# Optimization experiments

Measured on AMD Instinct MI355X. Metric: run time of the kernel, lower is better.

## Reference

```python
import jax, jax.numpy as jnp
import numpy as np

B, S, D = 2, 4096, 768
H = 12
HD = D // H  # 64
SCALE = HD ** -0.5


def setup_inputs() -> dict:
    key = jax.random.key(0)
    ks = jax.random.split(key, 5)
    return {
        "x": jax.random.normal(ks[0], (B, S, D), dtype=jnp.float32),
        "qkv_w": jax.random.normal(ks[1], (D, 3 * D), dtype=jnp.float32) * (D ** -0.5),
        "qkv_b": jax.random.normal(ks[2], (3 * D,), dtype=jnp.float32) * 0.02,
        "proj_w": jax.random.normal(ks[3], (D, D), dtype=jnp.float32) * (D ** -0.5),
        "proj_b": jax.random.normal(ks[4], (D,), dtype=jnp.float32) * 0.02,
    }


def reference(x, qkv_w, qkv_b, proj_w, proj_b):
    b, s, d = x.shape
    qkv = x @ qkv_w + qkv_b                      # [B, S, 3D]
    qkv = qkv.reshape(b, s, 3, H, HD)
    q, k, v = jnp.moveaxis(qkv, 2, 0)            # each [B, S, H, HD]
    q = jnp.swapaxes(q, 1, 2)                    # [B, H, S, HD]
    k = jnp.swapaxes(k, 1, 2)
    v = jnp.swapaxes(v, 1, 2)
    attn = jnp.einsum("bhqd,bhkd->bhqk", q, k) * SCALE  # [B, H, S, S]
    attn = jax.nn.softmax(attn, axis=-1)
    out = jnp.einsum("bhqk,bhkd->bhqd", attn, v)        # [B, H, S, HD]
    out = jnp.swapaxes(out, 1, 2).reshape(b, s, d)      # [B, S, D]
    return out @ proj_w + proj_b
```

## Files before the change

kernel.cpp:

```cpp
#include <hip/hip_runtime.h>

typedef unsigned short u16;
typedef __attribute__((ext_vector_type(8))) short bf16x8;
typedef __attribute__((ext_vector_type(4))) float f32x4;
typedef __attribute__((ext_vector_type(16))) float f32x16;

__device__ __forceinline__ u16 f2bf(float f) {
  union { float f; unsigned u; } v; v.f = f;
  unsigned r = v.u + 0x7fffu + ((v.u >> 16) & 1u);
  return (u16)(r >> 16);
}

__device__ __forceinline__ bf16x8 ld_frag(const char* p) {
  union { uint4 u; bf16x8 v; } t;
  t.u = *(const uint4*)p;
  return t.v;
}

__global__ __launch_bounds__(256) void k_prep(const float* __restrict__ x,
                                              const float* __restrict__ qkv_w,
                                              const float* __restrict__ proj_w,
                                              u16* __restrict__ xb,
                                              u16* __restrict__ wt,
                                              u16* __restrict__ pwt) {
  int bid = blockIdx.x, tid = threadIdx.x;
  if (bid < 6144) {
    int i = bid * 256 + tid;
    float4 v = ((const float4*)x)[i];
    ushort4 o; o.x = f2bf(v.x); o.y = f2bf(v.y); o.z = f2bf(v.z); o.w = f2bf(v.w);
    ((ushort4*)xb)[i] = o;
    return;
  }
  __shared__ float tile[32][33];
  const float* in; u16* out; int R, C, bx, by;
  if (bid < 6144 + 1728) {
    int t = bid - 6144; in = qkv_w; out = wt; R = 768; C = 2304;
    bx = (t % 72) * 32; by = (t / 72) * 32;
  } else {
    int t = bid - 7872; in = proj_w; out = pwt; R = 768; C = 768;
    bx = (t % 24) * 32; by = (t / 24) * 32;
  }
  int tx = tid & 31, ty = tid >> 5;
#pragma unroll
  for (int j = 0; j < 32; j += 8)
    tile[ty + j][tx] = in[(size_t)(by + ty + j) * C + bx + tx];
  __syncthreads();
#pragma unroll
  for (int j = 0; j < 32; j += 8)
    out[(size_t)(bx + ty + j) * R + by + tx] = f2bf(tile[tx][ty + j]);
}

#define GAS(p) ((const __attribute__((address_space(1))) void*)(p))
#define LAS(p) ((__attribute__((address_space(3))) void*)(p))

__global__ __launch_bounds__(256) void k_gemm_qkv(
    const u16* __restrict__ A,
    const u16* __restrict__ Bt,
    const float* __restrict__ bias,
    u16* __restrict__ Qb, u16* __restrict__ Kb, u16* __restrict__ Vb) {
  const int K = 768;
  __shared__ u16 Al[128 * 64];
  __shared__ u16 Bl[128 * 64];
  int tn0 = blockIdx.x * 128, tm0 = blockIdx.y * 128;
  int tid = threadIdx.x, w = tid >> 6, lane = tid & 63;
  int l16 = lane & 15, lg = lane >> 4;
  int wm = (w >> 1) * 64, wn = (w & 1) * 64;
  f32x4 acc[4][4];
#pragma unroll
  for (int fm = 0; fm < 4; ++fm)
#pragma unroll
    for (int fn = 0; fn < 4; ++fn) acc[fm][fn] = (f32x4){0.f, 0.f, 0.f, 0.f};
  int srow = w * 32 + (lane >> 3);
  int scol = (lane & 7) * 8;
  for (int k0 = 0; k0 < K; k0 += 64) {
#pragma unroll
    for (int i = 0; i < 4; ++i) {
      __builtin_amdgcn_global_load_lds(GAS(A + (size_t)(tm0 + srow + i * 8) * K + k0 + scol),
                                       LAS((char*)Al + w * 4096 + i * 1024 + lane * 16), 16, 0, 0);
      __builtin_amdgcn_global_load_lds(GAS(Bt + (size_t)(tn0 + srow + i * 8) * K + k0 + scol),
                                       LAS((char*)Bl + w * 4096 + i * 1024 + lane * 16), 16, 0, 0);
    }
    __syncthreads();
#pragma unroll
    for (int ks = 0; ks < 2; ++ks) {
      bf16x8 af[4], bv[4];
#pragma unroll
      for (int f = 0; f < 4; ++f)
        af[f] = *(const bf16x8*)&Al[(wm + f * 16 + l16) * 64 + lg * 8 + ks * 32];
#pragma unroll
      for (int f = 0; f < 4; ++f)
        bv[f] = *(const bf16x8*)&Bl[(wn + f * 16 + l16) * 64 + lg * 8 + ks * 32];
#pragma unroll
      for (int fm = 0; fm < 4; ++fm)
#pragma unroll
        for (int fn = 0; fn < 4; ++fn)
          acc[fm][fn] = __builtin_amdgcn_mfma_f32_16x16x32_bf16(af[fm], bv[fn], acc[fm][fn], 0, 0, 0);
    }
    __syncthreads();
  }
  int part = tn0 / 768;
  u16* dst = part == 0 ? Qb : (part == 1 ? Kb : Vb);
  float qscale = (part == 0) ? 0.18033688011112042f : 1.0f;
#pragma unroll
  for (int fn = 0; fn < 4; ++fn) {
    int nn = tn0 + wn + fn * 16 + l16;
    float bvs = bias[nn];
    int np = nn - part * 768;
    int hh = np >> 6, hd = np & 63;
#pragma unroll
    for (int fm = 0; fm < 4; ++fm) {
#pragma unroll
      for (int r = 0; r < 4; ++r) {
        int m = tm0 + wm + fm * 16 + lg * 4 + r;
        int bb = m >> 12, s = m & 4095;
        size_t idx;
        if (part == 2) {
          int sp = (s & ~12) | ((s & 8) >> 1) | ((s & 4) << 1);
          idx = (((size_t)(bb * 12 + hh)) * 64 + hd) * 4096 + sp;
        } else {
          idx = (((size_t)(bb * 12 + hh)) * 4096 + s) * 64 + hd;
        }
        dst[idx] = f2bf((acc[fm][fn][r] + bvs) * qscale);
      }
    }
  }
}

__global__ __launch_bounds__(256) void k_gemm_proj(
    const u16* __restrict__ A,
    const u16* __restrict__ Bt,
    const float* __restrict__ bias, float* __restrict__ out) {
  const int K = 768;
  __shared__ u16 Al[128 * 64];
  __shared__ u16 Bl[128 * 64];
  int tn0 = blockIdx.x * 128, tm0 = blockIdx.y * 128;
  int tid = threadIdx.x, w = tid >> 6, lane = tid & 63;
  int l16 = lane & 15, lg = lane >> 4;
  int wm = (w >> 1) * 64, wn = (w & 1) * 64;
  f32x4 acc[4][4];
#pragma unroll
  for (int fm = 0; fm < 4; ++fm)
#pragma unroll
    for (int fn = 0; fn < 4; ++fn) acc[fm][fn] = (f32x4){0.f, 0.f, 0.f, 0.f};
  int srow = w * 32 + (lane >> 3);
  int scol = (lane & 7) * 8;
  for (int k0 = 0; k0 < K; k0 += 64) {
#pragma unroll
    for (int i = 0; i < 4; ++i) {
      __builtin_amdgcn_global_load_lds(GAS(A + (size_t)(tm0 + srow + i * 8) * K + k0 + scol),
                                       LAS((char*)Al + w * 4096 + i * 1024 + lane * 16), 16, 0, 0);
      __builtin_amdgcn_global_load_lds(GAS(Bt + (size_t)(tn0 + srow + i * 8) * K + k0 + scol),
                                       LAS((char*)Bl + w * 4096 + i * 1024 + lane * 16), 16, 0, 0);
    }
    __syncthreads();
#pragma unroll
    for (int ks = 0; ks < 2; ++ks) {
      bf16x8 af[4], bv[4];
#pragma unroll
      for (int f = 0; f < 4; ++f)
        af[f] = *(const bf16x8*)&Al[(wm + f * 16 + l16) * 64 + lg * 8 + ks * 32];
#pragma unroll
      for (int f = 0; f < 4; ++f)
        bv[f] = *(const bf16x8*)&Bl[(wn + f * 16 + l16) * 64 + lg * 8 + ks * 32];
#pragma unroll
      for (int fm = 0; fm < 4; ++fm)
#pragma unroll
        for (int fn = 0; fn < 4; ++fn)
          acc[fm][fn] = __builtin_amdgcn_mfma_f32_16x16x32_bf16(af[fm], bv[fn], acc[fm][fn], 0, 0, 0);
    }
    __syncthreads();
  }
#pragma unroll
  for (int fn = 0; fn < 4; ++fn) {
    int nn = tn0 + wn + fn * 16 + l16;
    float bvs = bias[nn];
#pragma unroll
    for (int fm = 0; fm < 4; ++fm) {
#pragma unroll
      for (int r = 0; r < 4; ++r) {
        int m = tm0 + wm + fm * 16 + lg * 4 + r;
        out[(size_t)m * 768 + nn] = acc[fm][fn][r] + bvs;
      }
    }
  }
}

__global__ __launch_bounds__(256, 3) void k_attn(const u16* __restrict__ Qb,
                                                 const u16* __restrict__ Kb,
                                                 const u16* __restrict__ Vtg,
                                                 u16* __restrict__ Ob) {
  const int S = 4096, NH = 12, D = 768;
  __shared__ u16 Kl[2][64 * 64];
  __shared__ u16 Vl[2][64 * 64];

  int bid0 = blockIdx.x;
  int bid = (bid0 & 7) * 96 + (bid0 >> 3);
  int qp = bid & 31;
  int bh = bid >> 5;
  int b = bh / NH, h = bh % NH;
  int rot = ((bid0 >> 8) * 21) & 63;
  const u16* Qh = Qb + (size_t)bh * S * 64;
  const char* Khc = (const char*)(Kb + (size_t)bh * S * 64);
  const char* Vhc = (const char*)(Vtg + (size_t)bh * 64 * S);

  int tid = threadIdx.x, w = tid >> 6, lane = tid & 63;
  int q31 = lane & 31, hi = lane >> 5;
  int swb = (q31 & 7) << 4;
  int coff = (hi << 4);

  unsigned xoff[4];
#pragma unroll
  for (int ks = 0; ks < 4; ++ks)
    xoff[ks] = (unsigned)(q31 * 128 + ((ks * 32 + coff) ^ swb));

  int r8 = lane >> 3;
  int chs = (lane & 7) ^ r8;
  const char* kSrc = Khc + (size_t)(w * 16 + r8) * 128 + chs * 16;
  const char* vSrc = Vhc + (size_t)(w * 16 + r8) * 8192 + chs * 16;
  char* kDst0 = (char*)&Kl[0][0] + w * 2048 + lane * 16;
  char* vDst0 = (char*)&Vl[0][0] + w * 2048 + lane * 16;

  auto STAGE = [&](int bufi, int kv) {
#pragma unroll
    for (int qq = 0; qq < 2; ++qq) {
      __builtin_amdgcn_global_load_lds(GAS(kSrc + (size_t)kv * 8192 + qq * 1024),
                                       LAS(kDst0 + bufi * 8192 + qq * 1024), 16, 0, 0);
      __builtin_amdgcn_global_load_lds(GAS(vSrc + (size_t)qq * 65536 + (size_t)kv * 128),
                                       LAS(vDst0 + bufi * 8192 + qq * 1024), 16, 0, 0);
    }
  };

  int qbase = qp * 128 + w * 32;
  const u16* qrow = Qh + (size_t)(qbase + q31) * 64;
  bf16x8 qf[4];
#pragma unroll
  for (int ks = 0; ks < 4; ++ks)
    qf[ks] = *(const bf16x8*)(qrow + ks * 16 + hi * 8);

  f32x16 of0, of1, la0, la1;
#pragma unroll
  for (int i = 0; i < 16; ++i) { of0[i] = 0.f; of1[i] = 0.f; la0[i] = 0.f; la1[i] = 0.f; }

  auto TILE = [&](const char* KB, const char* VB) {
    f32x16 s0, s1;
#pragma unroll
    for (int i = 0; i < 16; ++i) { s0[i] = 0.f; s1[i] = 0.f; }
    __builtin_amdgcn_s_setprio(1);
#pragma unroll
    for (int ks = 0; ks < 4; ++ks) {
      bf16x8 kf = ld_frag(KB + xoff[ks]);
      s0 = __builtin_amdgcn_mfma_f32_32x32x16_bf16(kf, qf[ks], s0, 0, 0, 0);
    }
#pragma unroll
    for (int ks = 0; ks < 4; ++ks) {
      bf16x8 kf = ld_frag(KB + 4096 + xoff[ks]);
      s1 = __builtin_amdgcn_mfma_f32_32x32x16_bf16(kf, qf[ks], s1, 0, 0, 0);
    }
    __builtin_amdgcn_s_setprio(0);
#pragma unroll
    for (int i = 0; i < 16; ++i) {
      s0[i] = __builtin_amdgcn_exp2f(s0[i]);
      s1[i] = __builtin_amdgcn_exp2f(s1[i]);
    }
    la0 += s0;
    la1 += s1;
    union U8 { unsigned u[4]; bf16x8 v; };
    bf16x8 pf[4];
#define MK_PF(DST, SS, R0)                                                        \
    { U8 tt;                                                                      \
      asm("v_cvt_pk_bf16_f32 %0,%1,%2" : "=v"(tt.u[0]) : "v"(SS[R0+0]), "v"(SS[R0+1])); \
      asm("v_cvt_pk_bf16_f32 %0,%1,%2" : "=v"(tt.u[1]) : "v"(SS[R0+2]), "v"(SS[R0+3])); \
      asm("v_cvt_pk_bf16_f32 %0,%1,%2" : "=v"(tt.u[2]) : "v"(SS[R0+4]), "v"(SS[R0+5])); \
      asm("v_cvt_pk_bf16_f32 %0,%1,%2" : "=v"(tt.u[3]) : "v"(SS[R0+6]), "v"(SS[R0+7])); \
      DST = tt.v; }
    MK_PF(pf[0], s0, 0); MK_PF(pf[1], s0, 8);
    MK_PF(pf[2], s1, 0); MK_PF(pf[3], s1, 8);
#undef MK_PF
    __builtin_amdgcn_s_setprio(1);
#pragma unroll
    for (int ks = 0; ks < 4; ++ks) {
      bf16x8 vf = ld_frag(VB + xoff[ks]);
      of0 = __builtin_amdgcn_mfma_f32_32x32x16_bf16(vf, pf[ks], of0, 0, 0, 0);
    }
#pragma unroll
    for (int ks = 0; ks < 4; ++ks) {
      bf16x8 vf = ld_frag(VB + 4096 + xoff[ks]);
      of1 = __builtin_amdgcn_mfma_f32_32x32x16_bf16(vf, pf[ks], of1, 0, 0, 0);
    }
    __builtin_amdgcn_s_setprio(0);
  };

  const char* K0 = (const char*)&Kl[0][0];
  const char* K1 = (const char*)&Kl[1][0];
  const char* V0 = (const char*)&Vl[0][0];
  const char* V1 = (const char*)&Vl[1][0];

  STAGE(0, rot);
  __syncthreads();

#pragma unroll 1
  for (int kv = 0; kv < S / 64; kv += 2) {
    STAGE(1, (kv + 1 + rot) & 63);
    TILE(K0, V0);
    __syncthreads();
    if (kv + 2 < S / 64) STAGE(0, (kv + 2 + rot) & 63);
    TILE(K1, V1);
    if (kv + 2 < S / 64) __syncthreads();
  }

  float ts[8];
#pragma unroll
  for (int i = 0; i < 8; ++i) ts[i] = (la0[i] + la0[i + 8]) + (la1[i] + la1[i + 8]);
#pragma unroll
  for (int st = 4; st >= 1; st >>= 1)
#pragma unroll
    for (int i = 0; i < 4; ++i)
      if (i < st) ts[i] += ts[i + st];
  float l_full = ts[0] + __shfl_xor(ts[0], 32, 64);
  float inv = 1.f / l_full;
  int q = qbase + q31;
  u16* orow = Ob + (size_t)(b * S + q) * D + h * 64;
#pragma unroll
  for (int g = 0; g < 4; ++g) {
    ushort4 o0, o1;
    o0.x = f2bf(of0[g * 4 + 0] * inv); o0.y = f2bf(of0[g * 4 + 1] * inv);
    o0.z = f2bf(of0[g * 4 + 2] * inv); o0.w = f2bf(of0[g * 4 + 3] * inv);
    o1.x = f2bf(of1[g * 4 + 0] * inv); o1.y = f2bf(of1[g * 4 + 1] * inv);
    o1.z = f2bf(of1[g * 4 + 2] * inv); o1.w = f2bf(of1[g * 4 + 3] * inv);
    int hd0 = g * 8 + hi * 4;
    *(ushort4*)(orow + hd0) = o0;
    *(ushort4*)(orow + 32 + hd0) = o1;
  }
}

extern "C" void kernel_launch(void* const* d_in, const int* in_sizes, int n_in,
                              void* d_out, int out_size, void* d_ws, size_t ws_size,
                              hipStream_t stream) {
  const float* x      = (const float*)d_in[0];
  const float* qkv_w  = (const float*)d_in[1];
  const float* qkv_b  = (const float*)d_in[2];
  const float* proj_w = (const float*)d_in[3];
  const float* proj_b = (const float*)d_in[4];
  float* out = (float*)d_out;

  u16* ws  = (u16*)d_ws;
  u16* xb  = ws;
  u16* wt  = xb + 8192 * 768;
  u16* pwt = wt + 2304 * 768;
  u16* Qb  = pwt + 768 * 768;
  u16* Kb  = Qb + 24 * 4096 * 64;
  u16* Vt  = Kb + 24 * 4096 * 64;
  u16* Ob  = Vt + 24 * 4096 * 64;

  k_prep<<<8448, 256, 0, stream>>>(x, qkv_w, proj_w, xb, wt, pwt);
  k_gemm_qkv<<<dim3(18, 64), 256, 0, stream>>>(xb, wt, qkv_b, Qb, Kb, Vt);
  k_attn<<<768, 256, 0, stream>>>(Qb, Kb, Vt, Ob);
  k_gemm_proj<<<dim3(6, 64), 256, 0, stream>>>(Ob, pwt, proj_b, out);
}
```

Baseline: 221.6 us.

## Stage QKV epilogue through LDS for coalesced stores; halve proj GEMM M-tile

```diff
diff --git a/kernel.cpp b/kernel.cpp
--- a/kernel.cpp
+++ b/kernel.cpp
@@ -59,8 +59,10 @@
     const float* __restrict__ bias,
     u16* __restrict__ Qb, u16* __restrict__ Kb, u16* __restrict__ Vb) {
   const int K = 768;
-  __shared__ u16 Al[128 * 64];
-  __shared__ u16 Bl[128 * 64];
+  __shared__ __align__(16) char SMEM[34816];
+  u16* Al = (u16*)SMEM;
+  u16* Bl = (u16*)(SMEM + 16384);
+  u16* P  = (u16*)SMEM;
   int tn0 = blockIdx.x * 128, tm0 = blockIdx.y * 128;
   int tid = threadIdx.x, w = tid >> 6, lane = tid & 63;
   int l16 = lane & 15, lg = lane >> 4;
@@ -99,30 +101,59 @@
     __syncthreads();
   }
   int part = tn0 / 768;
-  u16* dst = part == 0 ? Qb : (part == 1 ? Kb : Vb);
   float qscale = (part == 0) ? 0.18033688011112042f : 1.0f;
-#pragma unroll
-  for (int fn = 0; fn < 4; ++fn) {
-    int nn = tn0 + wn + fn * 16 + l16;
-    float bvs = bias[nn];
-    int np = nn - part * 768;
-    int hh = np >> 6, hd = np & 63;
-#pragma unroll
-    for (int fm = 0; fm < 4; ++fm) {
-#pragma unroll
-      for (int r = 0; r < 4; ++r) {
-        int m = tm0 + wm + fm * 16 + lg * 4 + r;
-        int bb = m >> 12, s = m & 4095;
-        size_t idx;
-        if (part == 2) {
-          int sp = (s & ~12) | ((s & 8) >> 1) | ((s & 4) << 1);
-          idx = (((size_t)(bb * 12 + hh)) * 64 + hd) * 4096 + sp;
-        } else {
-          idx = (((size_t)(bb * 12 + hh)) * 4096 + s) * 64 + hd;
+
+  if (part == 2) {
+    int lgp = ((lg & 1) << 3) | ((lg & 2) << 1);
+#pragma unroll
+    for (int fn = 0; fn < 4; ++fn) {
+      int n = wn + fn * 16 + l16;
+      float bvs = bias[tn0 + n];
+#pragma unroll
+      for (int fm = 0; fm < 4; ++fm) {
+        int mp = wm + fm * 16 + lgp;
+        ushort4 hv;
+        hv.x = f2bf(acc[fm][fn][0] + bvs);
+        hv.y = f2bf(acc[fm][fn][1] + bvs);
+        hv.z = f2bf(acc[fm][fn][2] + bvs);
+        hv.w = f2bf(acc[fm][fn][3] + bvs);
+        *(ushort4*)&P[n * 136 + mp] = hv;
+      }
+    }
+    __syncthreads();
+    int n = tid >> 1, mc = tid & 1;
+    int np = (tn0 - 1536) + n;
+    int bh2 = (tm0 >> 12) * 12 + (np >> 6);
+    int hd = np & 63;
+    u16* g = Vb + ((size_t)bh2 * 64 + hd) * 4096 + (tm0 & 4095) + mc * 64;
+    const u16* lp = P + n * 136 + mc * 64;
+#pragma unroll
+    for (int j = 0; j < 8; ++j)
+      ((uint4*)g)[j] = ((const uint4*)lp)[j];
+  } else {
+#pragma unroll
+    for (int fn = 0; fn < 4; ++fn) {
+      int n = wn + fn * 16 + l16;
+      float bvs = bias[tn0 + n];
+#pragma unroll
+      for (int fm = 0; fm < 4; ++fm)
+#pragma unroll
+        for (int r = 0; r < 4; ++r) {
+          int m = wm + fm * 16 + lg * 4 + r;
+          P[m * 136 + n] = f2bf((acc[fm][fn][r] + bvs) * qscale);
         }
-        dst[idx] = f2bf((acc[fm][fn][r] + bvs) * qscale);
-      }
-    }
+    }
+    __syncthreads();
+    u16* dst = part == 0 ? Qb : Kb;
+    int m = tid >> 1, hh2 = tid & 1;
+    int mg = tm0 + m;
+    int np0 = tn0 - part * 768;
+    int bh2 = (mg >> 12) * 12 + (np0 >> 6) + hh2;
+    u16* g = dst + ((size_t)bh2 * 4096 + (mg & 4095)) * 64;
+    const u16* lp = P + m * 136 + hh2 * 64;
+#pragma unroll
+    for (int j = 0; j < 8; ++j)
+      ((uint4*)g)[j] = ((const uint4*)lp)[j];
   }
 }
 
@@ -131,39 +162,40 @@
     const u16* __restrict__ Bt,
     const float* __restrict__ bias, float* __restrict__ out) {
   const int K = 768;
-  __shared__ u16 Al[128 * 64];
+  __shared__ u16 Al[64 * 64];
   __shared__ u16 Bl[128 * 64];
-  int tn0 = blockIdx.x * 128, tm0 = blockIdx.y * 128;
+  int tn0 = blockIdx.x * 128, tm0 = blockIdx.y * 64;
   int tid = threadIdx.x, w = tid >> 6, lane = tid & 63;
   int l16 = lane & 15, lg = lane >> 4;
-  int wm = (w >> 1) * 64, wn = (w & 1) * 64;
-  f32x4 acc[4][4];
-#pragma unroll
-  for (int fm = 0; fm < 4; ++fm)
+  int wm = (w >> 1) * 32, wn = (w & 1) * 64;
+  f32x4 acc[2][4];
+#pragma unroll
+  for (int fm = 0; fm < 2; ++fm)
 #pragma unroll
     for (int fn = 0; fn < 4; ++fn) acc[fm][fn] = (f32x4){0.f, 0.f, 0.f, 0.f};
-  int srow = w * 32 + (lane >> 3);
-  int scol = (lane & 7) * 8;
+  int srow = tid >> 3;
+  int scol = (tid & 7) * 8;
   for (int k0 = 0; k0 < K; k0 += 64) {
 #pragma unroll
-    for (int i = 0; i < 4; ++i) {
-      __builtin_amdgcn_global_load_lds(GAS(A + (size_t)(tm0 + srow + i * 8) * K + k0 + scol),
-                                       LAS((char*)Al + w * 4096 + i * 1024 + lane * 16), 16, 0, 0);
-      __builtin_amdgcn_global_load_lds(GAS(Bt + (size_t)(tn0 + srow + i * 8) * K + k0 + scol),
-                                       LAS((char*)Bl + w * 4096 + i * 1024 + lane * 16), 16, 0, 0);
-    }
+    for (int i = 0; i < 2; ++i)
+      __builtin_amdgcn_global_load_lds(GAS(A + (size_t)(tm0 + i * 32 + srow) * K + k0 + scol),
+                                       LAS((char*)Al + i * 4096 + tid * 16), 16, 0, 0);
+#pragma unroll
+    for (int i = 0; i < 4; ++i)
+      __builtin_amdgcn_global_load_lds(GAS(Bt + (size_t)(tn0 + i * 32 + srow) * K + k0 + scol),
+                                       LAS((char*)Bl + i * 4096 + tid * 16), 16, 0, 0);
     __syncthreads();
 #pragma unroll
     for (int ks = 0; ks < 2; ++ks) {
-      bf16x8 af[4], bv[4];
-#pragma unroll
-      for (int f = 0; f < 4; ++f)
+      bf16x8 af[2], bv[4];
+#pragma unroll
+      for (int f = 0; f < 2; ++f)
         af[f] = *(const bf16x8*)&Al[(wm + f * 16 + l16) * 64 + lg * 8 + ks * 32];
 #pragma unroll
       for (int f = 0; f < 4; ++f)
         bv[f] = *(const bf16x8*)&Bl[(wn + f * 16 + l16) * 64 + lg * 8 + ks * 32];
 #pragma unroll
-      for (int fm = 0; fm < 4; ++fm)
+      for (int fm = 0; fm < 2; ++fm)
 #pragma unroll
         for (int fn = 0; fn < 4; ++fn)
           acc[fm][fn] = __builtin_amdgcn_mfma_f32_16x16x32_bf16(af[fm], bv[fn], acc[fm][fn], 0, 0, 0);
@@ -175,7 +207,7 @@
     int nn = tn0 + wn + fn * 16 + l16;
     float bvs = bias[nn];
 #pragma unroll
-    for (int fm = 0; fm < 4; ++fm) {
+    for (int fm = 0; fm < 2; ++fm) {
 #pragma unroll
       for (int r = 0; r < 4; ++r) {
         int m = tm0 + wm + fm * 16 + lg * 4 + r;
@@ -355,5 +387,5 @@
   k_prep<<<8448, 256, 0, stream>>>(x, qkv_w, proj_w, xb, wt, pwt);
   k_gemm_qkv<<<dim3(18, 64), 256, 0, stream>>>(xb, wt, qkv_b, Qb, Kb, Vt);
   k_attn<<<768, 256, 0, stream>>>(Qb, Kb, Vt, Ob);
-  k_gemm_proj<<<dim3(6, 64), 256, 0, stream>>>(Ob, pwt, proj_b, out);
-}
+  k_gemm_proj<<<dim3(6, 128), 256, 0, stream>>>(Ob, pwt, proj_b, out);
+}
```

Result: faster. 212.5 us (-4.1%).
